# Performance work log

Measured on AMD Instinct MI355X. Metric: run time of the kernel, lower is better.

Reference implementation:

```python
import jax, jax.numpy as jnp
import numpy as np

EMBED = 1024
HEADS = 16
HEAD_DIM = EMBED // HEADS
N, L = 4, 2048


def setup_inputs() -> dict:
    key = jax.random.key(0)
    ks = jax.random.split(key, 12)
    s = 1.0 / np.sqrt(EMBED)
    return {
        "query": jax.random.normal(ks[0], (N, L, EMBED), jnp.float32),
        "attn_bias": jax.random.normal(ks[1], (1, HEADS, L, L), jnp.float32),
        "mask": jax.random.randint(ks[2], (N, L), 0, 2) > 0,  # True = masked key
        "Wq": jax.random.normal(ks[3], (EMBED, EMBED), jnp.float32) * s,
        "bq": jnp.zeros((EMBED,), jnp.float32),
        "Wk": jax.random.normal(ks[4], (EMBED, EMBED), jnp.float32) * s,
        "bk": jnp.zeros((EMBED,), jnp.float32),
        "Wv": jax.random.normal(ks[5], (EMBED, EMBED), jnp.float32) * s,
        "bv": jnp.zeros((EMBED,), jnp.float32),
        "Wo": jax.random.normal(ks[6], (EMBED, EMBED), jnp.float32) * s,
        "bo": jnp.zeros((EMBED,), jnp.float32),
    }


def _split_heads(x):
    n, l, _ = x.shape
    return x.reshape(n, l, HEADS, HEAD_DIM).transpose(0, 2, 1, 3)  # [N,H,L,D]


def reference(query, attn_bias, mask, Wq, bq, Wk, bk, Wv, bv, Wo, bo):
    scaling = HEAD_DIM ** -0.5
    v = _split_heads(query @ Wv.T + bv)
    k = _split_heads(query @ Wk.T + bk)
    q = _split_heads((query @ Wq.T + bq) * scaling)

    scores = jnp.einsum("bhqd,bhkd->bhqk", q, k) + attn_bias
    # mask [N, k_len] -> [N, 1, 1, k_len]; True positions get -inf
    scores = jnp.where(mask[:, None, None, :], -jnp.inf, scores)
    attn_weights = jax.nn.softmax(scores, axis=-1)  # [N,H,L,L]
    attn_weights_avg = attn_weights.mean(axis=1)     # [N,L,L]
    # dropout p=0.0 -> identity
    attn = jnp.einsum("bhqk,bhkd->bhqd", attn_weights, v)
    attn = attn.transpose(0, 2, 1, 3).reshape(query.shape[0], query.shape[1], EMBED)
    out = attn @ Wo.T + bo
    return out, attn_weights_avg
```

## Files before the change

kernel.cpp:

```cpp
#include <hip/hip_runtime.h>
#include <stdint.h>

typedef __bf16 bf16;
typedef __bf16 bf16x4 __attribute__((ext_vector_type(4)));
typedef __bf16 bf16x8 __attribute__((ext_vector_type(8)));
typedef float f32x4 __attribute__((ext_vector_type(4)));

#define MFMA16(a, b, c) __builtin_amdgcn_mfma_f32_16x16x32_bf16((a), (b), (c), 0, 0, 0)

static constexpr int NB = 4;
static constexpr int NH = 16;
static constexpr int SL = 2048;
static constexpr int HD = 64;
static constexpr int ED = 1024;
static constexpr int MR = NB * SL;

__device__ __forceinline__ void gl_lds16(const void* g, void* l) {
    __builtin_amdgcn_global_load_lds(
        (const __attribute__((address_space(1))) unsigned int*)g,
        (__attribute__((address_space(3))) unsigned int*)l, 16, 0, 0);
}

__global__ void k_split(const float* __restrict__ src, bf16* __restrict__ hi,
                        bf16* __restrict__ lo, int n4) {
    int i = blockIdx.x * blockDim.x + threadIdx.x;
    if (i >= n4) return;
    const float4 v = ((const float4*)src)[i];
    float vv[4] = {v.x, v.y, v.z, v.w};
    bf16x4 hv, lv;
#pragma unroll
    for (int e = 0; e < 4; ++e) {
        bf16 h = (bf16)vv[e];
        hv[e] = h;
        lv[e] = (bf16)(vv[e] - (float)h);
    }
    ((bf16x4*)hi)[i] = hv;
    ((bf16x4*)lo)[i] = lv;
}

__global__ void k_cast(const float* __restrict__ src, bf16* __restrict__ dst, int n4) {
    int i = blockIdx.x * blockDim.x + threadIdx.x;
    if (i >= n4) return;
    const float4 v = ((const float4*)src)[i];
    bf16x4 hv = {(bf16)v.x, (bf16)v.y, (bf16)v.z, (bf16)v.w};
    ((bf16x4*)dst)[i] = hv;
}

__global__ void k_mlg(const float* __restrict__ mrow, const float* __restrict__ srow,
                      float* __restrict__ mlg, int n) {
    int i = blockIdx.x * blockDim.x + threadIdx.x;
    if (i < n) mlg[i] = mrow[i] + __logf(16.0f * srow[i]);
}

__global__ __launch_bounds__(256) void k_qkv_gemm(
    const bf16* __restrict__ xh, const bf16* __restrict__ wh,
    const float* __restrict__ bq, const float* __restrict__ bk,
    const float* __restrict__ bv,
    bf16* __restrict__ qh, bf16* __restrict__ kh, bf16* __restrict__ vh)
{
    __shared__ __attribute__((aligned(16))) bf16 As[128 * 32];
    __shared__ __attribute__((aligned(16))) bf16 Bs[128 * 32];

    const int z  = blockIdx.z;
    const int m0 = blockIdx.x * 128;
    const int n0 = blockIdx.y * 128;
    const int tid = threadIdx.x, wave = tid >> 6, lane = tid & 63;
    const int wr = wave >> 1, wc = wave & 1;
    const int fr = lane & 15, fq = lane >> 4;
    const bf16* Wh = wh + (size_t)z * ED * ED;

    const f32x4 z4 = {0.f, 0.f, 0.f, 0.f};
    f32x4 acc[4][4];
#pragma unroll
    for (int i = 0; i < 4; ++i)
#pragma unroll
        for (int j = 0; j < 4; ++j) acc[i][j] = z4;

#pragma unroll 1
    for (int kk = 0; kk < ED; kk += 32) {
#pragma unroll
        for (int r = 0; r < 2; ++r) {
            const int chunk = r * 256 + tid;
            const int row = chunk >> 2, c8 = (chunk & 3) * 8;
            const size_t ax = (size_t)(m0 + row) * ED + kk + c8;
            const size_t bx = (size_t)(n0 + row) * ED + kk + c8;
            const int db = (r * 256 + wave * 64) * 8;
            gl_lds16(xh + ax, &As[db]);
            gl_lds16(Wh + bx, &Bs[db]);
        }
        __syncthreads();
        bf16x8 af[4], bfg[4];
#pragma unroll
        for (int i = 0; i < 4; ++i) {
            const int arow = wr * 64 + i * 16 + fr;
            af[i] = *(const bf16x8*)&As[arow * 32 + fq * 8];
            const int brow = wc * 64 + i * 16 + fr;
            bfg[i] = *(const bf16x8*)&Bs[brow * 32 + fq * 8];
        }
#pragma unroll
        for (int mi = 0; mi < 4; ++mi)
#pragma unroll
            for (int ni = 0; ni < 4; ++ni)
                acc[mi][ni] = MFMA16(af[mi], bfg[ni], acc[mi][ni]);
        __syncthreads();
    }

    const float* bias = (z == 0) ? bq : (z == 1) ? bk : bv;
#pragma unroll
    for (int mi = 0; mi < 4; ++mi) {
#pragma unroll
        for (int ni = 0; ni < 4; ++ni) {
            const int col = n0 + wc * 64 + ni * 16 + fr;
            const int hh = col >> 6, dd = col & 63;
#pragma unroll
            for (int j = 0; j < 4; ++j) {
                const int row = m0 + wr * 64 + mi * 16 + fq * 4 + j;
                float v = acc[mi][ni][j] + bias[col];
                const int nb = row >> 11, li = row & (SL - 1);
                const size_t off = (((size_t)nb * NH + hh) * SL + li) * HD + dd;
                if (z == 0) {
                    qh[off] = (bf16)(v * 0.125f);
                } else if (z == 1) {
                    kh[off] = (bf16)v;
                } else {
                    vh[off] = (bf16)v;
                }
            }
        }
    }
}

__global__ __launch_bounds__(256) void k_out_gemm(
    const bf16* __restrict__ ah,
    const bf16* __restrict__ wh, const bf16* __restrict__ wl,
    const float* __restrict__ bo, float* __restrict__ out)
{
    __shared__ __attribute__((aligned(16))) bf16 As[128 * 32];
    __shared__ __attribute__((aligned(16))) bf16 Bs[2][128 * 32];

    const int m0 = blockIdx.x * 128;
    const int n0 = blockIdx.y * 128;
    const int tid = threadIdx.x, wave = tid >> 6, lane = tid & 63;
    const int wr = wave >> 1, wc = wave & 1;
    const int fr = lane & 15, fq = lane >> 4;

    const f32x4 z4 = {0.f, 0.f, 0.f, 0.f};
    f32x4 acc[4][4];
#pragma unroll
    for (int i = 0; i < 4; ++i)
#pragma unroll
        for (int j = 0; j < 4; ++j) acc[i][j] = z4;

#pragma unroll 1
    for (int kk = 0; kk < ED; kk += 32) {
#pragma unroll
        for (int r = 0; r < 2; ++r) {
            const int chunk = r * 256 + tid;
            const int row = chunk >> 2, c8 = (chunk & 3) * 8;
            const size_t ax = (size_t)(m0 + row) * ED + kk + c8;
            const size_t bx = (size_t)(n0 + row) * ED + kk + c8;
            const int db = (r * 256 + wave * 64) * 8;
            gl_lds16(ah + ax, &As[db]);
            gl_lds16(wh + bx, &Bs[0][db]);
            gl_lds16(wl + bx, &Bs[1][db]);
        }
        __syncthreads();
        bf16x8 af[4], bfg[4][2];
#pragma unroll
        for (int i = 0; i < 4; ++i) {
            const int arow = wr * 64 + i * 16 + fr;
            af[i] = *(const bf16x8*)&As[arow * 32 + fq * 8];
            const int brow = wc * 64 + i * 16 + fr;
            bfg[i][0] = *(const bf16x8*)&Bs[0][brow * 32 + fq * 8];
            bfg[i][1] = *(const bf16x8*)&Bs[1][brow * 32 + fq * 8];
        }
#pragma unroll
        for (int mi = 0; mi < 4; ++mi)
#pragma unroll
            for (int ni = 0; ni < 4; ++ni) {
                acc[mi][ni] = MFMA16(af[mi], bfg[ni][0], acc[mi][ni]);
                acc[mi][ni] = MFMA16(af[mi], bfg[ni][1], acc[mi][ni]);
            }
        __syncthreads();
    }

#pragma unroll
    for (int mi = 0; mi < 4; ++mi)
#pragma unroll
        for (int ni = 0; ni < 4; ++ni) {
            const int col = n0 + wc * 64 + ni * 16 + fr;
#pragma unroll
            for (int j = 0; j < 4; ++j) {
                const int row = m0 + wr * 64 + mi * 16 + fq * 4 + j;
                out[(size_t)row * ED + col] = acc[mi][ni][j] + bo[col];
            }
        }
}

__global__ __launch_bounds__(256) void k_flash(
    const bf16* __restrict__ qh, const bf16* __restrict__ kh,
    const bf16* __restrict__ vh,
    const float* __restrict__ bias, const int* __restrict__ mask,
    bf16* __restrict__ ch,
    float* __restrict__ mrow, float* __restrict__ srow)
{
    __shared__ __attribute__((aligned(16))) bf16 Ks[2][64 * 64];
    __shared__ __attribute__((aligned(16))) bf16 Vs[2][64 * 64];
    __shared__ __attribute__((aligned(16))) bf16 Ws[4][16 * 64];

    const int bid = blockIdx.x;
    const int xcd = bid & 7, local = bid >> 3;
    const int h = xcd * 2 + (local >> 6);
    const int rem = local & 63;
    const int qt = rem >> 2, n = rem & 3;

    const int tid = threadIdx.x, wave = tid >> 6, lane = tid & 63;
    const int fr = lane & 15, fq = lane >> 4;
    const int frx = fr & 7;
    const int q0 = qt * 128;
    const int qw = q0 + wave * 32;
    const size_t hoff = ((size_t)n * NH + h) * SL * HD;
    const f32x4 z4 = {0.f, 0.f, 0.f, 0.f};

    bf16x8 qf0[2], qf1[2];
#pragma unroll
    for (int m = 0; m < 2; ++m) {
        const size_t qb = hoff + (size_t)(qw + m * 16 + fr) * HD + fq * 8;
        qf0[m] = *(const bf16x8*)(qh + qb);
        qf1[m] = *(const bf16x8*)(qh + qb + 32);
    }

    f32x4 o[2][4];
#pragma unroll
    for (int m = 0; m < 2; ++m)
#pragma unroll
        for (int f = 0; f < 4; ++f) o[m][f] = z4;
    float mj[2][4], sj[2][4];
#pragma unroll
    for (int m = 0; m < 2; ++m)
#pragma unroll
        for (int j = 0; j < 4; ++j) { mj[m][j] = -3e38f; sj[m][j] = 0.f; }

    const int* mkb = mask + n * SL;
    const float* bh = bias + (size_t)h * SL * SL;

#pragma unroll
    for (int i = 0; i < 2; ++i) {
        const int li = i * 256 + tid;
        const int r = li >> 3, s = li & 7;
        gl_lds16(kh + hoff + (size_t)r * HD + (s ^ (r & 7)) * 8,
                 &Ks[0][(i * 256 + wave * 64) * 8]);
    }
    bf16x8 vr0 = *(const bf16x8*)(vh + hoff + (size_t)lane * HD + wave * 8);
    bf16x8 vr1 = *(const bf16x8*)(vh + hoff + (size_t)lane * HD + (wave + 4) * 8);
#pragma unroll
    for (int e = 0; e < 8; ++e) {
        const int d0 = wave * 8 + e, d1 = (wave + 4) * 8 + e;
        Vs[0][d0 * 64 + (((lane >> 3) ^ (d0 & 7)) << 3) + (lane & 7)] = vr0[e];
        Vs[0][d1 * 64 + (((lane >> 3) ^ (d1 & 7)) << 3) + (lane & 7)] = vr1[e];
    }
    vr0 = *(const bf16x8*)(vh + hoff + (size_t)(64 + lane) * HD + wave * 8);
    vr1 = *(const bf16x8*)(vh + hoff + (size_t)(64 + lane) * HD + (wave + 4) * 8);
    __syncthreads();

#pragma unroll 1
    for (int kt = 0; kt < 32; ++kt) {
        const int cur = kt & 1, nxt = cur ^ 1;
        const int kp1 = (kt < 31) ? kt + 1 : 31;
        const int kp2 = (kt < 30) ? kt + 2 : 31;

        const int mw0 = mkb[kt * 64 + fr];
        const int mw1 = mkb[kt * 64 + 16 + fr];
        const int mw2 = mkb[kt * 64 + 32 + fr];
        const int mw3 = mkb[kt * 64 + 48 + fr];

#pragma unroll
        for (int e = 0; e < 8; ++e) {
            const int d0 = wave * 8 + e, d1 = (wave + 4) * 8 + e;
            Vs[nxt][d0 * 64 + (((lane >> 3) ^ (d0 & 7)) << 3) + (lane & 7)] = vr0[e];
            Vs[nxt][d1 * 64 + (((lane >> 3) ^ (d1 & 7)) << 3) + (lane & 7)] = vr1[e];
        }
#pragma unroll
        for (int i = 0; i < 2; ++i) {
            const int li = i * 256 + tid;
            const int r = li >> 3, s = li & 7;
            gl_lds16(kh + hoff + (size_t)(kp1 * 64 + r) * HD + (s ^ (r & 7)) * 8,
                     &Ks[nxt][(i * 256 + wave * 64) * 8]);
        }
        vr0 = *(const bf16x8*)(vh + hoff + (size_t)(kp2 * 64 + lane) * HD + wave * 8);
        vr1 = *(const bf16x8*)(vh + hoff + (size_t)(kp2 * 64 + lane) * HD + (wave + 4) * 8);
        const int mbits = (mw0 != 0 ? 1 : 0) | (mw1 != 0 ? 2 : 0)
                        | (mw2 != 0 ? 4 : 0) | (mw3 != 0 ? 8 : 0);

#pragma unroll
        for (int m = 0; m < 2; ++m) {
            float bfr[4][4];
#pragma unroll
            for (int nf = 0; nf < 4; ++nf)
#pragma unroll
                for (int j = 0; j < 4; ++j)
                    bfr[nf][j] = bh[(size_t)(qw + m * 16 + fq * 4 + j) * SL
                                    + kt * 64 + nf * 16 + fr];

            f32x4 sf[4];
            __builtin_amdgcn_s_setprio(1);
#pragma unroll
            for (int nf = 0; nf < 4; ++nf) {
                const bf16* kp = &Ks[cur][(nf * 16 + fr) * 64];
                const bf16x8 b0 = *(const bf16x8*)&kp[(fq ^ frx) * 8];
                const bf16x8 b1 = *(const bf16x8*)&kp[((fq + 4) ^ frx) * 8];
                f32x4 a = z4;
                a = MFMA16(qf0[m], b0, a);
                a = MFMA16(qf1[m], b1, a);
                sf[nf] = a;
            }
            __builtin_amdgcn_s_setprio(0);

#pragma unroll
            for (int nf = 0; nf < 4; ++nf) {
                const bool mk = (mbits >> nf) & 1;
#pragma unroll
                for (int j = 0; j < 4; ++j) {
                    float s = sf[nf][j] + bfr[nf][j];
                    sf[nf][j] = mk ? -1e30f : s;
                }
            }

            float tmax[4];
#pragma unroll
            for (int j = 0; j < 4; ++j)
                tmax[j] = fmaxf(fmaxf(sf[0][j], sf[1][j]), fmaxf(sf[2][j], sf[3][j]));
            bool need = false;
#pragma unroll
            for (int j = 0; j < 4; ++j)
                need = need || (tmax[j] > mj[m][j] + 8.0f);
            if (__any(need)) {
#pragma unroll
                for (int d = 1; d < 16; d <<= 1)
#pragma unroll
                    for (int j = 0; j < 4; ++j)
                        tmax[j] = fmaxf(tmax[j], __shfl_xor(tmax[j], d));
#pragma unroll
                for (int j = 0; j < 4; ++j) {
                    const float mn = fmaxf(mj[m][j], tmax[j]);
                    const float scale = __expf(mj[m][j] - mn);
                    mj[m][j] = mn;
                    sj[m][j] *= scale;
#pragma unroll
                    for (int f = 0; f < 4; ++f) o[m][f][j] *= scale;
                }
            }
#pragma unroll
            for (int nf = 0; nf < 4; ++nf)
#pragma unroll
                for (int j = 0; j < 4; ++j) {
                    const float w = __expf(sf[nf][j] - mj[m][j]);
                    sf[nf][j] = w;
                    sj[m][j] += w;
                }

#pragma unroll
            for (int nf = 0; nf < 4; ++nf)
#pragma unroll
                for (int j = 0; j < 4; ++j) {
                    const int row = fq * 4 + j, col = nf * 16 + fr;
                    Ws[wave][row * 64 + (((col >> 3) ^ (row & 7)) << 3) + (fr & 7)] =
                        (bf16)sf[nf][j];
                }
            const bf16* wp = &Ws[wave][fr * 64];
            const bf16x8 wa0 = *(const bf16x8*)&wp[(fq ^ frx) * 8];
            const bf16x8 wa1 = *(const bf16x8*)&wp[((fq + 4) ^ frx) * 8];
            __builtin_amdgcn_s_setprio(1);
#pragma unroll
            for (int f = 0; f < 4; ++f) {
                const bf16* vp = &Vs[cur][(f * 16 + fr) * 64];
                const bf16x8 vb0 = *(const bf16x8*)&vp[(fq ^ frx) * 8];
                const bf16x8 vb1 = *(const bf16x8*)&vp[((fq + 4) ^ frx) * 8];
                o[m][f] = MFMA16(wa0, vb0, o[m][f]);
                o[m][f] = MFMA16(wa1, vb1, o[m][f]);
            }
            __builtin_amdgcn_s_setprio(0);
        }

        __syncthreads();
    }

#pragma unroll
    for (int m = 0; m < 2; ++m)
#pragma unroll
        for (int d = 1; d < 16; d <<= 1)
#pragma unroll
            for (int j = 0; j < 4; ++j)
                sj[m][j] += __shfl_xor(sj[m][j], d);

#pragma unroll
    for (int m = 0; m < 2; ++m) {
#pragma unroll
        for (int j = 0; j < 4; ++j) {
            const float inv = 1.0f / sj[m][j];
            const int row = n * SL + qw + m * 16 + fq * 4 + j;
#pragma unroll
            for (int f = 0; f < 4; ++f) {
                const float v = o[m][f][j] * inv;
                const size_t off = (size_t)row * ED + h * HD + f * 16 + fr;
                ch[off] = (bf16)v;
            }
        }
        if (fr == 0) {
#pragma unroll
            for (int j = 0; j < 4; ++j) {
                const int r = qw + m * 16 + fq * 4 + j;
                mrow[((size_t)n * NH + h) * SL + r] = mj[m][j];
                srow[((size_t)n * NH + h) * SL + r] = sj[m][j];
            }
        }
    }
}

__global__ __launch_bounds__(256) void k_avg(
    const bf16* __restrict__ qh, const bf16* __restrict__ kh,
    const float* __restrict__ bias, const int* __restrict__ mask,
    const float* __restrict__ mlg, float* __restrict__ avg)
{
    __shared__ __attribute__((aligned(16))) bf16 Ks2[2][64 * 64];

    const int qt = blockIdx.x, kt = blockIdx.y;
    const int tid = threadIdx.x, wave = tid >> 6, lane = tid & 63;
    const int fr = lane & 15, fq = lane >> 4;
    const int frx = fr & 7;
    const int q0 = qt * 64, k0 = kt * 64;
    const int qr = q0 + wave * 16;
    const f32x4 z4 = {0.f, 0.f, 0.f, 0.f};

    f32x4 acc[4][4];
#pragma unroll
    for (int nn = 0; nn < 4; ++nn)
#pragma unroll
        for (int nf = 0; nf < 4; ++nf) acc[nn][nf] = z4;

    int mkbits = 0;
#pragma unroll
    for (int nn = 0; nn < 4; ++nn)
#pragma unroll
        for (int nf = 0; nf < 4; ++nf)
            mkbits |= (mask[nn * SL + k0 + nf * 16 + fr] != 0 ? 1 : 0) << (nn * 4 + nf);

    auto stageK = [&](int hh, int nn2, int b) {
        const bf16* kb = kh + (((size_t)nn2 * NH + hh) * SL + k0) * HD;
#pragma unroll
        for (int i = 0; i < 2; ++i) {
            const int li = i * 256 + tid;
            const int r = li >> 3, s = li & 7;
            gl_lds16(kb + (size_t)r * HD + (s ^ (r & 7)) * 8,
                     &Ks2[b][(i * 256 + wave * 64) * 8]);
        }
    };
    auto loadQ = [&](int hh, int nn2, bf16x8& a0, bf16x8& a1) {
        const bf16* qb = qh + ((((size_t)nn2 * NH + hh) * SL + qr + fr) * HD) + fq * 8;
        a0 = *(const bf16x8*)qb;
        a1 = *(const bf16x8*)(qb + 32);
    };
    auto loadMlg = [&](int hh, int nn2) -> f32x4 {
        return *(const f32x4*)(mlg + ((size_t)nn2 * NH + hh) * SL + qr + fq * 4);
    };

    stageK(0, 0, 0);
    bf16x8 qcA, qcB;
    loadQ(0, 0, qcA, qcB);
    f32x4 mlgc = loadMlg(0, 0);
    __syncthreads();

#pragma unroll 1
    for (int h = 0; h < NH; ++h) {
        float bfr[4][4];
#pragma unroll
        for (int nf = 0; nf < 4; ++nf)
#pragma unroll
            for (int j = 0; j < 4; ++j)
                bfr[nf][j] = bias[((size_t)h * SL + qr + fq * 4 + j) * SL + k0 + nf * 16 + fr];

#pragma unroll
        for (int nn = 0; nn < 4; ++nn) {
            const int ih = h * 4 + nn;
            const int buf = ih & 1;

            bf16x8 qnA, qnB;
            f32x4 mlgn = mlgc;
            if (ih < 63) {
                const int jh = (ih + 1) >> 2, jnn = (ih + 1) & 3;
                stageK(jh, jnn, buf ^ 1);
                loadQ(jh, jnn, qnA, qnB);
                mlgn = loadMlg(jh, jnn);
            } else {
                qnA = qcA; qnB = qcB;
            }

#pragma unroll
            for (int nf = 0; nf < 4; ++nf) {
                const bf16* kp = &Ks2[buf][(nf * 16 + fr) * 64];
                const bf16x8 b0 = *(const bf16x8*)&kp[(fq ^ frx) * 8];
                const bf16x8 b1 = *(const bf16x8*)&kp[((fq + 4) ^ frx) * 8];
                f32x4 a = z4;
                a = MFMA16(qcA, b0, a);
                a = MFMA16(qcB, b1, a);
                const bool mk = (mkbits >> (nn * 4 + nf)) & 1;
#pragma unroll
                for (int j = 0; j < 4; ++j) {
                    const float w = mk ? 0.f
                        : __expf(a[j] + bfr[nf][j] - mlgc[j]);
                    acc[nn][nf][j] += w;
                }
            }
            __syncthreads();
            qcA = qnA; qcB = qnB; mlgc = mlgn;
        }
    }

#pragma unroll
    for (int nn = 0; nn < 4; ++nn)
#pragma unroll
        for (int j = 0; j < 4; ++j) {
            const size_t rowoff = ((size_t)nn * SL + qr + fq * 4 + j) * SL;
#pragma unroll
            for (int nf = 0; nf < 4; ++nf)
                avg[rowoff + k0 + nf * 16 + fr] = acc[nn][nf][j];
        }
}

extern "C" void kernel_launch(void* const* d_in, const int* in_sizes, int n_in,
                              void* d_out, int out_size, void* d_ws, size_t ws_size,
                              hipStream_t stream)
{
    (void)in_sizes; (void)n_in; (void)out_size; (void)ws_size;
    const float* query = (const float*)d_in[0];
    const float* bias  = (const float*)d_in[1];
    const int* mask = (const int*)d_in[2];
    const float* Wq = (const float*)d_in[3];
    const float* bq = (const float*)d_in[4];
    const float* Wk = (const float*)d_in[5];
    const float* bk = (const float*)d_in[6];
    const float* Wv = (const float*)d_in[7];
    const float* bv = (const float*)d_in[8];
    const float* Wo = (const float*)d_in[9];
    const float* bo = (const float*)d_in[10];
    float* out0 = (float*)d_out;
    float* out1 = out0 + (size_t)MR * ED;

    char* p = (char*)d_ws;
    auto carve = [&](size_t bytes) {
        char* r = p;
        p += (bytes + 255) & ~(size_t)255;
        return r;
    };
    const size_t QKVB = (size_t)NB * NH * SL * HD * 2;
    bf16* xh = (bf16*)carve((size_t)MR * ED * 2);
    bf16* wqkv = (bf16*)carve((size_t)3 * ED * ED * 2);
    bf16* woh = (bf16*)carve((size_t)ED * ED * 2);
    bf16* wol = (bf16*)carve((size_t)ED * ED * 2);
    bf16* qh = (bf16*)carve(QKVB);
    bf16* kh = (bf16*)carve(QKVB);
    bf16* vh = (bf16*)carve(QKVB);
    float* mrow = (float*)carve((size_t)NB * NH * SL * 4);
    float* srow = (float*)carve((size_t)NB * NH * SL * 4);
    float* mlg  = (float*)carve((size_t)NB * NH * SL * 4);
    bf16* ch = (bf16*)carve((size_t)MR * ED * 2);

    {
        const int n4 = MR * ED / 4;
        k_cast<<<(n4 + 255) / 256, 256, 0, stream>>>(query, xh, n4);
        const int w4 = ED * ED / 4;
        const float* Ws3[3] = {Wq, Wk, Wv};
        for (int i = 0; i < 3; ++i)
            k_cast<<<(w4 + 255) / 256, 256, 0, stream>>>(
                Ws3[i], wqkv + (size_t)i * ED * ED, w4);
        k_split<<<(w4 + 255) / 256, 256, 0, stream>>>(Wo, woh, wol, w4);
    }
    k_qkv_gemm<<<dim3(MR / 128, ED / 128, 3), 256, 0, stream>>>(
        xh, wqkv, bq, bk, bv, qh, kh, vh);
    k_flash<<<dim3(1024), 256, 0, stream>>>(
        qh, kh, vh, bias, mask, ch, mrow, srow);
    {
        const int nst = NB * NH * SL;
        k_mlg<<<(nst + 255) / 256, 256, 0, stream>>>(mrow, srow, mlg, nst);
    }
    k_avg<<<dim3(SL / 64, SL / 64), 256, 0, stream>>>(
        qh, kh, bias, mask, mlg, out1);
    k_out_gemm<<<dim3(MR / 128, ED / 128), 256, 0, stream>>>(
        ch, woh, wol, bo, out0);
}
```

Before: 510.5 us.

## Pre-transpose V and stage V and bias tiles via async LDS loads

Adds a kernel that transposes V into a [d, key] layout so the flash kernel can stage V tiles with direct global-to-LDS loads, like K, instead of register loads followed by scattered LDS writes. In the averaging kernel, per-head bias tiles are now double-buffered into shared memory with async loads rather than read per thread into registers. The aim is to cut VGPR pressure and LDS store work and to overlap bias fetches with compute. The cost is an extra kernel launch, another V-sized buffer with its write and read traffic, and 32KB more LDS in k_avg, which may lower occupancy.

```diff
diff --git a/kernel.cpp b/kernel.cpp
--- a/kernel.cpp
+++ b/kernel.cpp
@@ -50,6 +50,33 @@
                       float* __restrict__ mlg, int n) {
     int i = blockIdx.x * blockDim.x + threadIdx.x;
     if (i < n) mlg[i] = mrow[i] + __logf(16.0f * srow[i]);
+}
+
+__global__ __launch_bounds__(256) void k_vt(const bf16* __restrict__ v,
+                                            bf16* __restrict__ vt) {
+    __shared__ bf16 T[256 * 72];
+    const int n = blockIdx.z, h = blockIdx.y, kc = blockIdx.x * 256;
+    const int tid = threadIdx.x;
+    const size_t base1 = ((size_t)n * NH + h) * SL * HD;
+    const size_t base2 = ((size_t)n * NH + h) * HD * SL;
+
+#pragma unroll
+    for (int ri = 0; ri < 8; ++ri) {
+        const int kl = ri * 32 + (tid >> 3), d0 = (tid & 7) * 8;
+        const bf16x8 x = *(const bf16x8*)(v + base1 + (size_t)(kc + kl) * HD + d0);
+        *(bf16x8*)&T[kl * 72 + d0] = x;
+    }
+    __syncthreads();
+
+    const int d = tid >> 2, kch = (tid & 3) * 64;
+#pragma unroll
+    for (int i = 0; i < 8; ++i) {
+        bf16x8 y;
+#pragma unroll
+        for (int e = 0; e < 8; ++e)
+            y[e] = T[(kch + i * 8 + e) * 72 + d];
+        *(bf16x8*)(vt + base2 + (size_t)d * SL + kc + kch + i * 8) = y;
+    }
 }
 
 __global__ __launch_bounds__(256) void k_qkv_gemm(
@@ -199,7 +226,7 @@
 
 __global__ __launch_bounds__(256) void k_flash(
     const bf16* __restrict__ qh, const bf16* __restrict__ kh,
-    const bf16* __restrict__ vh,
+    const bf16* __restrict__ vt,
     const float* __restrict__ bias, const int* __restrict__ mask,
     bf16* __restrict__ ch,
     float* __restrict__ mrow, float* __restrict__ srow)
@@ -244,51 +271,41 @@
     const int* mkb = mask + n * SL;
     const float* bh = bias + (size_t)h * SL * SL;
 
-#pragma unroll
-    for (int i = 0; i < 2; ++i) {
-        const int li = i * 256 + tid;
-        const int r = li >> 3, s = li & 7;
-        gl_lds16(kh + hoff + (size_t)r * HD + (s ^ (r & 7)) * 8,
-                 &Ks[0][(i * 256 + wave * 64) * 8]);
-    }
-    bf16x8 vr0 = *(const bf16x8*)(vh + hoff + (size_t)lane * HD + wave * 8);
-    bf16x8 vr1 = *(const bf16x8*)(vh + hoff + (size_t)lane * HD + (wave + 4) * 8);
-#pragma unroll
-    for (int e = 0; e < 8; ++e) {
-        const int d0 = wave * 8 + e, d1 = (wave + 4) * 8 + e;
-        Vs[0][d0 * 64 + (((lane >> 3) ^ (d0 & 7)) << 3) + (lane & 7)] = vr0[e];
-        Vs[0][d1 * 64 + (((lane >> 3) ^ (d1 & 7)) << 3) + (lane & 7)] = vr1[e];
-    }
-    vr0 = *(const bf16x8*)(vh + hoff + (size_t)(64 + lane) * HD + wave * 8);
-    vr1 = *(const bf16x8*)(vh + hoff + (size_t)(64 + lane) * HD + (wave + 4) * 8);
+    auto stageK = [&](int kt2, int b) {
+#pragma unroll
+        for (int i = 0; i < 2; ++i) {
+            const int li = i * 256 + tid;
+            const int r = li >> 3, s = li & 7;
+            gl_lds16(kh + hoff + (size_t)(kt2 * 64 + r) * HD + (s ^ (r & 7)) * 8,
+                     &Ks[b][(i * 256 + wave * 64) * 8]);
+        }
+    };
+    auto stageV = [&](int kt2, int b) {
+#pragma unroll
+        for (int i = 0; i < 2; ++i) {
+            const int li = i * 256 + tid;
+            const int r = li >> 3, s = li & 7;
+            gl_lds16(vt + hoff + (size_t)r * SL + kt2 * 64 + (s ^ (r & 7)) * 8,
+                     &Vs[b][(i * 256 + wave * 64) * 8]);
+        }
+    };
+
+    stageK(0, 0);
+    stageV(0, 0);
     __syncthreads();
 
 #pragma unroll 1
     for (int kt = 0; kt < 32; ++kt) {
         const int cur = kt & 1, nxt = cur ^ 1;
         const int kp1 = (kt < 31) ? kt + 1 : 31;
-        const int kp2 = (kt < 30) ? kt + 2 : 31;
 
         const int mw0 = mkb[kt * 64 + fr];
         const int mw1 = mkb[kt * 64 + 16 + fr];
         const int mw2 = mkb[kt * 64 + 32 + fr];
         const int mw3 = mkb[kt * 64 + 48 + fr];
 
-#pragma unroll
-        for (int e = 0; e < 8; ++e) {
-            const int d0 = wave * 8 + e, d1 = (wave + 4) * 8 + e;
-            Vs[nxt][d0 * 64 + (((lane >> 3) ^ (d0 & 7)) << 3) + (lane & 7)] = vr0[e];
-            Vs[nxt][d1 * 64 + (((lane >> 3) ^ (d1 & 7)) << 3) + (lane & 7)] = vr1[e];
-        }
-#pragma unroll
-        for (int i = 0; i < 2; ++i) {
-            const int li = i * 256 + tid;
-            const int r = li >> 3, s = li & 7;
-            gl_lds16(kh + hoff + (size_t)(kp1 * 64 + r) * HD + (s ^ (r & 7)) * 8,
-                     &Ks[nxt][(i * 256 + wave * 64) * 8]);
-        }
-        vr0 = *(const bf16x8*)(vh + hoff + (size_t)(kp2 * 64 + lane) * HD + wave * 8);
-        vr1 = *(const bf16x8*)(vh + hoff + (size_t)(kp2 * 64 + lane) * HD + (wave + 4) * 8);
+        stageK(kp1, nxt);
+        stageV(kp1, nxt);
         const int mbits = (mw0 != 0 ? 1 : 0) | (mw1 != 0 ? 2 : 0)
                         | (mw2 != 0 ? 4 : 0) | (mw3 != 0 ? 8 : 0);
 
@@ -423,6 +440,7 @@
     const float* __restrict__ mlg, float* __restrict__ avg)
 {
     __shared__ __attribute__((aligned(16))) bf16 Ks2[2][64 * 64];
+    __shared__ __attribute__((aligned(16))) float Bs2[2][64 * 64];
 
     const int qt = blockIdx.x, kt = blockIdx.y;
     const int tid = threadIdx.x, wave = tid >> 6, lane = tid & 63;
@@ -453,6 +471,16 @@
             const int r = li >> 3, s = li & 7;
             gl_lds16(kb + (size_t)r * HD + (s ^ (r & 7)) * 8,
                      &Ks2[b][(i * 256 + wave * 64) * 8]);
+        }
+    };
+    auto stageB = [&](int hh, int b) {
+        const float* bb = bias + (size_t)hh * SL * SL + (size_t)q0 * SL + k0;
+#pragma unroll
+        for (int i = 0; i < 4; ++i) {
+            const int li = i * 256 + tid;
+            const int r = li >> 4, c = li & 15;
+            gl_lds16(bb + (size_t)r * SL + c * 4,
+                     &Bs2[b][(i * 256 + wave * 64) * 4]);
         }
     };
     auto loadQ = [&](int hh, int nn2, bf16x8& a0, bf16x8& a1) {
@@ -465,6 +493,7 @@
     };
 
     stageK(0, 0, 0);
+    stageB(0, 0);
     bf16x8 qcA, qcB;
     loadQ(0, 0, qcA, qcB);
     f32x4 mlgc = loadMlg(0, 0);
@@ -472,13 +501,7 @@
 
 #pragma unroll 1
     for (int h = 0; h < NH; ++h) {
-        float bfr[4][4];
-#pragma unroll
-        for (int nf = 0; nf < 4; ++nf)
-#pragma unroll
-            for (int j = 0; j < 4; ++j)
-                bfr[nf][j] = bias[((size_t)h * SL + qr + fq * 4 + j) * SL + k0 + nf * 16 + fr];
-
+        const int hb = h & 1;
 #pragma unroll
         for (int nn = 0; nn < 4; ++nn) {
             const int ih = h * 4 + nn;
@@ -494,6 +517,7 @@
             } else {
                 qnA = qcA; qnB = qcB;
             }
+            if (nn == 0 && h < NH - 1) stageB(h + 1, hb ^ 1);
 
 #pragma unroll
             for (int nf = 0; nf < 4; ++nf) {
@@ -507,7 +531,9 @@
 #pragma unroll
                 for (int j = 0; j < 4; ++j) {
                     const float w = mk ? 0.f
-                        : __expf(a[j] + bfr[nf][j] - mlgc[j]);
+                        : __expf(a[j] + Bs2[hb][(wave * 16 + fq * 4 + j) * 64
+                                                + nf * 16 + fr]
+                                 - mlgc[j]);
                     acc[nn][nf][j] += w;
                 }
             }
@@ -560,6 +586,7 @@
     bf16* qh = (bf16*)carve(QKVB);
     bf16* kh = (bf16*)carve(QKVB);
     bf16* vh = (bf16*)carve(QKVB);
+    bf16* vtb = (bf16*)carve(QKVB);
     float* mrow = (float*)carve((size_t)NB * NH * SL * 4);
     float* srow = (float*)carve((size_t)NB * NH * SL * 4);
     float* mlg  = (float*)carve((size_t)NB * NH * SL * 4);
@@ -577,8 +604,9 @@
     }
     k_qkv_gemm<<<dim3(MR / 128, ED / 128, 3), 256, 0, stream>>>(
         xh, wqkv, bq, bk, bv, qh, kh, vh);
+    k_vt<<<dim3(SL / 256, NH, NB), 256, 0, stream>>>(vh, vtb);
     k_flash<<<dim3(1024), 256, 0, stream>>>(
-        qh, kh, vh, bias, mask, ch, mrow, srow);
+        qh, kh, vtb, bias, mask, ch, mrow, srow);
     {
         const int nst = NB * NH * SL;
         k_mlg<<<(nst + 255) / 256, 256, 0, stream>>>(mrow, srow, mlg, nst);
```

New measurement: 582.9 us. 1.14x slower.
